# Performance work log

Hardware: AMD Instinct MI355X
Metric: run time of the kernel (lower is better)

The kernel has to match this reference:

```python
import jax, jax.numpy as jnp
import numpy as np

N_NODES = 100000
N_EDGES = 3200000
IN_FEATS = 16
OUT_FEATS = 2
K = 3


def setup_inputs() -> dict:
    key = jax.random.key(0)
    k1, k2, k3, k4 = jax.random.split(key, 4)
    in_feat = jax.random.normal(k1, (N_NODES, IN_FEATS), dtype=jnp.float32)
    # Linear(K*in_feats -> out_feats, bias=False) weight, torch layout (out, in)
    W = jax.random.normal(k2, (OUT_FEATS, K * IN_FEATS), dtype=jnp.float32) * (1.0 / np.sqrt(K * IN_FEATS))
    src = jax.random.randint(k3, (N_EDGES,), 0, N_NODES, dtype=jnp.int64)
    dst = jax.random.randint(k4, (N_EDGES,), 0, N_NODES, dtype=jnp.int64)
    # cached dgl.laplacian_lambda_max value; 2.0 is the normalized-Laplacian bound
    lambda_max = jnp.full((1,), 2.0, dtype=jnp.float32)
    return {"in_feat": in_feat, "W": W, "src": src, "dst": dst, "lambda_max": lambda_max}


def reference(in_feat, W, src, dst, lambda_max):
    N = in_feat.shape[0]
    # in-degree based symmetric normalization, clamp(min=1)
    deg = jax.ops.segment_sum(jnp.ones_like(dst, dtype=in_feat.dtype), dst, num_segments=N)
    norm = jnp.clip(deg, 1.0) ** -0.5  # (N,)
    norm = norm[:, None]
    re_norm = (2.0 / lambda_max)[None, :]  # (1,1), broadcasts over nodes

    def prop(x):
        # D^{-1/2} A D^{-1/2} x via gather from src, scatter-sum to dst
        m = (x * norm)[src]                                    # (E, d)
        return jax.ops.segment_sum(m, dst, num_segments=N) * norm

    X0 = in_feat
    X1 = -re_norm * prop(X0) + X0 * (re_norm - 1.0)
    X2 = -2.0 * re_norm * prop(X1) + X1 * (2.0 * (re_norm - 1.0)) - X0
    Xt = jnp.concatenate([X0, X1, X2], axis=1)                 # (N, K*d)
    h = Xt @ W.T                                               # (N, out)
    return jax.nn.relu(h)  # DGL ChebConv default activation
```

## Files before the change

kernel.cpp:

```cpp
#include <hip/hip_runtime.h>
#include <hip/hip_bf16.h>


#define NN   100000
#define NE   3200000
#define F    16
#define CB   128
#define NBUK 782
#define ECHK 8192
#define NBLK 391
#define LCAP 5120
#define HXW  1025
#define PCAP 4608

__device__ __forceinline__ float bflo(unsigned int u) {
    return __uint_as_float(u << 16);
}
__device__ __forceinline__ float bfhi(unsigned int u) {
    return __uint_as_float(u & 0xffff0000u);
}
__device__ __forceinline__ unsigned int f2bf(float f) {
    __hip_bfloat16 b = __float2bfloat16(f);
    return (unsigned int)*reinterpret_cast<unsigned short*>(&b);
}

__global__ __launch_bounds__(512) void k_lsort(const int* __restrict__ src,
        const int* __restrict__ dst, int* __restrict__ hxg, int* __restrict__ csort) {
    __shared__ int pk[ECHK];
    __shared__ int hx[HXW];
    __shared__ int cur[1024];
    __shared__ int csum[512];
    int t = threadIdx.x, blk = blockIdx.x;
    for (int j = t; j < 1024; j += 512) hx[j] = 0;
    __syncthreads();
    int s0 = blk * ECHK;
    int lim = min(s0 + ECHK, NE);
    for (int e = s0 + t; e < lim; e += 512)
        atomicAdd(&hx[dst[e] >> 7], 1);
    __syncthreads();
    int b0 = t * 2;
    int c0 = hx[b0], c1 = hx[b0 + 1];
    csum[t] = c0 + c1;
    __syncthreads();
    for (int o = 1; o < 512; o <<= 1) {
        int add = (t >= o) ? csum[t - o] : 0;
        __syncthreads();
        csum[t] += add;
        __syncthreads();
    }
    int ce = csum[t] - (c0 + c1);
    hx[b0] = ce;  hx[b0 + 1] = ce + c0;
    cur[b0] = ce; cur[b0 + 1] = ce + c0;
    if (t == 511) hx[1024] = csum[511];
    __syncthreads();
    for (int j = t; j < HXW; j += 512)
        hxg[blk * HXW + j] = hx[j];
    for (int e = s0 + t; e < lim; e += 512) {
        int d = dst[e];
        int pos = atomicAdd(&cur[d >> 7], 1);
        pk[pos] = (src[e] << 7) | (d & 127);
    }
    __syncthreads();
    int len = lim - s0;
    for (int i = t; i < len; i += 512)
        csort[s0 + i] = pk[i];
}

__global__ __launch_bounds__(512) void k_sort(const int* __restrict__ csort,
        const int* __restrict__ hxg, const float* __restrict__ X0,
        int* __restrict__ es, unsigned int* __restrict__ P,
        unsigned short* __restrict__ Y0, unsigned short* __restrict__ Y1) {
    __shared__ int pk[LCAP];
    __shared__ int pk2[LCAP];
    __shared__ int dsc[512];
    __shared__ int cnt[CB], loc[CB], cur[CB];
    __shared__ float nvs[CB];
    int b = blockIdx.x, t = threadIdx.x;
    int h0 = 0, c = 0;
    if (t < NBLK) {
        h0 = hxg[t * HXW + b];
        c  = hxg[t * HXW + b + 1] - h0;
    }
    dsc[t] = c;
    if (t < CB) cnt[t] = 0;
    if (b == 0 && t < 4) {
        ((uint2*)Y0)[(size_t)NN * 4 + t] = make_uint2(0u, 0u);
        ((uint2*)Y1)[(size_t)NN * 4 + t] = make_uint2(0u, 0u);
    }
    __syncthreads();
    for (int o = 1; o < 512; o <<= 1) {
        int add = (t >= o) ? dsc[t - o] : 0;
        __syncthreads();
        dsc[t] += add;
        __syncthreads();
    }
    int len = dsc[511];
    int dpos = dsc[t] - c;
    if (len > LCAP) len = LCAP;
    if (c > 0 && dpos < LCAP) {
        int rl = c;
        if (dpos + rl > LCAP) rl = LCAP - dpos;
        int sbase = t * ECHK + h0;
        for (int i = 0; i < rl; ++i)
            pk[dpos + i] = csort[sbase + i];
    }
    __syncthreads();
    for (int i = t; i < len; i += 512)
        atomicAdd(&cnt[pk[i] & 127], 1);
    __syncthreads();
    if (t < CB) loc[t] = cnt[t];
    __syncthreads();
    for (int o = 1; o < CB; o <<= 1) {
        int add = 0;
        if (t < CB && t >= o) add = loc[t - o];
        __syncthreads();
        if (t < CB) loc[t] += add;
        __syncthreads();
    }
    if (t < CB) {
        int excl = loc[t] - cnt[t];
        loc[t] = excl;
        cur[t] = excl;
        int n = b * CB + t;
        if (n < NN) {
            unsigned dg = cnt[t] > 1023 ? 1023u : (unsigned)cnt[t];
            P[n] = ((unsigned)(b * LCAP + excl) << 10) | dg;
            nvs[t] = rsqrtf((float)(cnt[t] < 1 ? 1 : cnt[t]));
        }
    }
    __syncthreads();
    for (int j = t; j < CB * 4; j += 512) {
        int dl = j >> 2;
        int n = b * CB + dl;
        if (n < NN) {
            float nv = nvs[dl];
            size_t g4 = (size_t)n * 4 + (j & 3);
            float4 x0 = ((const float4*)X0)[g4];
            uint2 o;
            o.x = f2bf(x0.x * nv) | (f2bf(x0.y * nv) << 16);
            o.y = f2bf(x0.z * nv) | (f2bf(x0.w * nv) << 16);
            ((uint2*)Y0)[g4] = o;
        }
    }
    for (int i = t; i < len; i += 512) {
        int p = pk[i];
        int pos = atomicAdd(&cur[p & 127], 1);
        pk2[pos] = p >> 7;
    }
    __syncthreads();
    for (int i = t; i < len; i += 512)
        es[b * LCAP + i] = pk2[i];
}

__global__ __launch_bounds__(256) void k_prop1(const unsigned int* __restrict__ P,
        const int* __restrict__ es, const unsigned short* __restrict__ Y0,
        const float* __restrict__ X0, const float* __restrict__ lm,
        unsigned short* __restrict__ Y1) {
    __shared__ int sidx[PCAP];
    int blk = blockIdx.x, t = threadIdx.x;
    int b = blk >> 1, half = blk & 1;
    int n0 = b * CB + half * 64;
    if (n0 >= NN) return;
    unsigned pk0 = P[n0];
    int nL = min(n0 + 63, NN - 1);
    unsigned pkL = P[nL];
    int st = (int)(pk0 >> 10);
    int en = (int)(pkL >> 10) + (int)(pkL & 1023u);
    int slen = en - st;
    if (slen > PCAP) slen = PCAP;
    for (int i = t; i < slen; i += 256)
        sidx[i] = es[st + i];
    __syncthreads();
    int n = n0 + (t >> 2), h = t & 3;
    if (n >= NN) return;
    unsigned pkn = P[n];
    int beg = (int)(pkn >> 10) - st;
    int dg = (int)(pkn & 1023u);
    int lend = min(beg + dg, slen);
    const uint2* Yv = (const uint2*)Y0;
    float a0 = 0.f, a1 = 0.f, a2 = 0.f, a3 = 0.f;
    for (int e0 = beg; e0 < lend; e0 += 8) {
#pragma unroll
        for (int j = 0; j < 8; ++j) {
            int sp = e0 + j;
            int s = (sp < lend) ? sidx[sp] : NN;
            uint2 u = Yv[(size_t)s * 4 + h];
            a0 += bflo(u.x); a1 += bfhi(u.x);
            a2 += bflo(u.y); a3 += bfhi(u.y);
        }
    }
    float nv = rsqrtf((float)(dg < 1 ? 1 : dg));
    float r  = 2.0f / lm[0];
    float k1 = -r * nv, k2 = r - 1.0f;
    int tid4 = n * 4 + h;
    float4 x0 = ((const float4*)X0)[tid4];
    float x1a = k1 * a0 + k2 * x0.x;
    float x1b = k1 * a1 + k2 * x0.y;
    float x1c = k1 * a2 + k2 * x0.z;
    float x1d = k1 * a3 + k2 * x0.w;
    uint2 o;
    o.x = f2bf(nv * x1a) | (f2bf(nv * x1b) << 16);
    o.y = f2bf(nv * x1c) | (f2bf(nv * x1d) << 16);
    ((uint2*)Y1)[tid4] = o;
}

__global__ __launch_bounds__(256) void k_prop2(const unsigned int* __restrict__ P,
        const int* __restrict__ es, const unsigned short* __restrict__ Y1,
        const float* __restrict__ X0, const float* __restrict__ lm,
        const float* __restrict__ W, float* __restrict__ out) {
    __shared__ int sidx[PCAP];
    __shared__ float Ws[96];
    int blk = blockIdx.x, t = threadIdx.x;
    int b = blk >> 1, half = blk & 1;
    int n0 = b * CB + half * 64;
    if (n0 >= NN) return;
    if (t < 96) Ws[t] = W[t];
    unsigned pk0 = P[n0];
    int nL = min(n0 + 63, NN - 1);
    unsigned pkL = P[nL];
    int st = (int)(pk0 >> 10);
    int en = (int)(pkL >> 10) + (int)(pkL & 1023u);
    int slen = en - st;
    if (slen > PCAP) slen = PCAP;
    for (int i = t; i < slen; i += 256)
        sidx[i] = es[st + i];
    __syncthreads();
    int n = n0 + (t >> 2), h = t & 3;
    if (n >= NN) return;
    unsigned pkn = P[n];
    int beg = (int)(pkn >> 10) - st;
    int dg = (int)(pkn & 1023u);
    int lend = min(beg + dg, slen);
    const uint2* Yv = (const uint2*)Y1;
    float a0 = 0.f, a1 = 0.f, a2 = 0.f, a3 = 0.f;
    for (int e0 = beg; e0 < lend; e0 += 8) {
#pragma unroll
        for (int j = 0; j < 8; ++j) {
            int sp = e0 + j;
            int s = (sp < lend) ? sidx[sp] : NN;
            uint2 u = Yv[(size_t)s * 4 + h];
            a0 += bflo(u.x); a1 += bfhi(u.x);
            a2 += bflo(u.y); a3 += bfhi(u.y);
        }
    }
    int dc = dg < 1 ? 1 : dg;
    float nv = rsqrtf((float)dc);
    float rn = sqrtf((float)dc);
    float r  = 2.0f / lm[0];
    int tid4 = n * 4 + h;
    float4 x0 = ((const float4*)X0)[tid4];
    uint2 uy = ((const uint2*)Y1)[tid4];
    float x1a = bflo(uy.x) * rn, x1b = bfhi(uy.x) * rn;
    float x1c = bflo(uy.y) * rn, x1d = bfhi(uy.y) * rn;
    float c1 = -2.0f * r * nv, c2 = 2.0f * (r - 1.0f);
    float x2a = c1 * a0 + c2 * x1a - x0.x;
    float x2b = c1 * a1 + c2 * x1b - x0.y;
    float x2c = c1 * a2 + c2 * x1c - x0.z;
    float x2d = c1 * a3 + c2 * x1d - x0.w;
    int f0 = 4 * h;
    float t0 = Ws[f0] * x0.x + Ws[f0 + 1] * x0.y + Ws[f0 + 2] * x0.z + Ws[f0 + 3] * x0.w
             + Ws[16 + f0] * x1a + Ws[17 + f0] * x1b + Ws[18 + f0] * x1c + Ws[19 + f0] * x1d
             + Ws[32 + f0] * x2a + Ws[33 + f0] * x2b + Ws[34 + f0] * x2c + Ws[35 + f0] * x2d;
    float t1 = Ws[48 + f0] * x0.x + Ws[49 + f0] * x0.y + Ws[50 + f0] * x0.z + Ws[51 + f0] * x0.w
             + Ws[64 + f0] * x1a + Ws[65 + f0] * x1b + Ws[66 + f0] * x1c + Ws[67 + f0] * x1d
             + Ws[80 + f0] * x2a + Ws[81 + f0] * x2b + Ws[82 + f0] * x2c + Ws[83 + f0] * x2d;
    t0 += __shfl_xor(t0, 2, 4); t0 += __shfl_xor(t0, 1, 4);
    t1 += __shfl_xor(t1, 2, 4); t1 += __shfl_xor(t1, 1, 4);
    if (h == 0) {
        out[(size_t)n * 2 + 0] = fmaxf(t0, 0.f);
        out[(size_t)n * 2 + 1] = fmaxf(t1, 0.f);
    }
}

extern "C" void kernel_launch(void* const* d_in, const int* in_sizes, int n_in,
                              void* d_out, int out_size, void* d_ws, size_t ws_size,
                              hipStream_t stream) {
    const float* X0  = (const float*)d_in[0];
    const float* W   = (const float*)d_in[1];
    const int*   src = (const int*)d_in[2];
    const int*   dst = (const int*)d_in[3];
    const float* lm  = (const float*)d_in[4];
    float* out = (float*)d_out;

    int*   hxg   = (int*)d_ws;
    int*   csort = hxg + (size_t)NBLK * HXW;
    int*   es    = csort + NE;
    unsigned int* P = (unsigned int*)(es + (size_t)NBUK * LCAP);
    unsigned short* Y0 = (unsigned short*)(P + NN);
    unsigned short* Y1 = Y0 + (size_t)(NN + 1) * F;

    k_lsort<<<NBLK, 512, 0, stream>>>(src, dst, hxg, csort);
    k_sort <<<NBUK, 512, 0, stream>>>(csort, hxg, X0, es, P, Y0, Y1);
    k_prop1<<<NBUK * 2, 256, 0, stream>>>(P, es, Y0, X0, lm, Y1);
    k_prop2<<<NBUK * 2, 256, 0, stream>>>(P, es, Y1, X0, lm, W, out);
}
```

Measured before the change: 175.1 us.

## Pad per-node edge lists to multiples of eight and vectorize index loads

Each node's sorted source list is now padded to a multiple of 8 with a sentinel index that points at a zero row, and offsets are stored in units of 8. The propagation kernels can then read indices as two int4 loads per group of 8 with no bounds checks. The sort kernel also drops the intermediate shared staging buffer and the 512-wide scan, reading csort twice directly from global memory instead. The costs are extra padded gather work, a larger LCAP footprint, and serial per-thread loops over csort.

```diff
diff --git a/kernel.cpp b/kernel.cpp
--- a/kernel.cpp
+++ b/kernel.cpp
@@ -9,7 +9,7 @@
 #define NBUK 782
 #define ECHK 8192
 #define NBLK 391
-#define LCAP 5120
+#define LCAP 5632
 #define HXW  1025
 #define PCAP 4608
 
@@ -70,45 +70,29 @@
         const int* __restrict__ hxg, const float* __restrict__ X0,
         int* __restrict__ es, unsigned int* __restrict__ P,
         unsigned short* __restrict__ Y0, unsigned short* __restrict__ Y1) {
-    __shared__ int pk[LCAP];
     __shared__ int pk2[LCAP];
-    __shared__ int dsc[512];
     __shared__ int cnt[CB], loc[CB], cur[CB];
     __shared__ float nvs[CB];
     int b = blockIdx.x, t = threadIdx.x;
-    int h0 = 0, c = 0;
-    if (t < NBLK) {
-        h0 = hxg[t * HXW + b];
-        c  = hxg[t * HXW + b + 1] - h0;
-    }
-    dsc[t] = c;
     if (t < CB) cnt[t] = 0;
     if (b == 0 && t < 4) {
         ((uint2*)Y0)[(size_t)NN * 4 + t] = make_uint2(0u, 0u);
         ((uint2*)Y1)[(size_t)NN * 4 + t] = make_uint2(0u, 0u);
     }
-    __syncthreads();
-    for (int o = 1; o < 512; o <<= 1) {
-        int add = (t >= o) ? dsc[t - o] : 0;
-        __syncthreads();
-        dsc[t] += add;
-        __syncthreads();
-    }
-    int len = dsc[511];
-    int dpos = dsc[t] - c;
-    if (len > LCAP) len = LCAP;
-    if (c > 0 && dpos < LCAP) {
-        int rl = c;
-        if (dpos + rl > LCAP) rl = LCAP - dpos;
-        int sbase = t * ECHK + h0;
-        for (int i = 0; i < rl; ++i)
-            pk[dpos + i] = csort[sbase + i];
-    }
-    __syncthreads();
-    for (int i = t; i < len; i += 512)
-        atomicAdd(&cnt[pk[i] & 127], 1);
-    __syncthreads();
-    if (t < CB) loc[t] = cnt[t];
+    int h0 = 0, rl = 0;
+    if (t < NBLK) {
+        h0 = hxg[t * HXW + b];
+        rl = hxg[t * HXW + b + 1] - h0;
+    }
+    int sbase = t * ECHK + h0;
+    __syncthreads();
+    for (int i = 0; i < rl; ++i) {
+        int p = csort[sbase + i];
+        atomicAdd(&cnt[p & 127], 1);
+    }
+    __syncthreads();
+    int pc = 0;
+    if (t < CB) { pc = (cnt[t] + 7) & ~7; loc[t] = pc; }
     __syncthreads();
     for (int o = 1; o < CB; o <<= 1) {
         int add = 0;
@@ -118,17 +102,29 @@
         __syncthreads();
     }
     if (t < CB) {
-        int excl = loc[t] - cnt[t];
+        int excl = loc[t] - pc;
         loc[t] = excl;
         cur[t] = excl;
         int n = b * CB + t;
         if (n < NN) {
-            unsigned dg = cnt[t] > 1023 ? 1023u : (unsigned)cnt[t];
-            P[n] = ((unsigned)(b * LCAP + excl) << 10) | dg;
+            unsigned dgc = cnt[t] > 1023 ? 1023u : (unsigned)cnt[t];
+            P[n] = ((unsigned)((b * LCAP + excl) >> 3) << 10) | dgc;
             nvs[t] = rsqrtf((float)(cnt[t] < 1 ? 1 : cnt[t]));
         }
     }
     __syncthreads();
+    int plen = loc[CB - 1] + ((cnt[CB - 1] + 7) & ~7);
+    if (plen > LCAP) plen = LCAP;
+    if (t < CB) {
+        int e0 = loc[t] + cnt[t];
+        int e1 = loc[t] + ((cnt[t] + 7) & ~7);
+        for (int i = e0; i < e1 && i < LCAP; ++i) pk2[i] = NN;
+    }
+    for (int i = 0; i < rl; ++i) {
+        int p = csort[sbase + i];
+        int pos = atomicAdd(&cur[p & 127], 1);
+        if (pos < LCAP) pk2[pos] = p >> 7;
+    }
     for (int j = t; j < CB * 4; j += 512) {
         int dl = j >> 2;
         int n = b * CB + dl;
@@ -142,13 +138,8 @@
             ((uint2*)Y0)[g4] = o;
         }
     }
-    for (int i = t; i < len; i += 512) {
-        int p = pk[i];
-        int pos = atomicAdd(&cur[p & 127], 1);
-        pk2[pos] = p >> 7;
-    }
-    __syncthreads();
-    for (int i = t; i < len; i += 512)
+    __syncthreads();
+    for (int i = t; i < plen; i += 512)
         es[b * LCAP + i] = pk2[i];
 }
 
@@ -156,7 +147,7 @@
         const int* __restrict__ es, const unsigned short* __restrict__ Y0,
         const float* __restrict__ X0, const float* __restrict__ lm,
         unsigned short* __restrict__ Y1) {
-    __shared__ int sidx[PCAP];
+    __shared__ __align__(16) int sidx[PCAP];
     int blk = blockIdx.x, t = threadIdx.x;
     int b = blk >> 1, half = blk & 1;
     int n0 = b * CB + half * 64;
@@ -164,8 +155,8 @@
     unsigned pk0 = P[n0];
     int nL = min(n0 + 63, NN - 1);
     unsigned pkL = P[nL];
-    int st = (int)(pk0 >> 10);
-    int en = (int)(pkL >> 10) + (int)(pkL & 1023u);
+    int st = (int)(pk0 >> 10) << 3;
+    int en = ((int)(pkL >> 10) << 3) + (int)(((pkL & 1023u) + 7u) & ~7u);
     int slen = en - st;
     if (slen > PCAP) slen = PCAP;
     for (int i = t; i < slen; i += 256)
@@ -174,20 +165,20 @@
     int n = n0 + (t >> 2), h = t & 3;
     if (n >= NN) return;
     unsigned pkn = P[n];
-    int beg = (int)(pkn >> 10) - st;
+    int beg = ((int)(pkn >> 10) << 3) - st;
     int dg = (int)(pkn & 1023u);
-    int lend = min(beg + dg, slen);
+    int nb = (dg + 7) >> 3;
     const uint2* Yv = (const uint2*)Y0;
     float a0 = 0.f, a1 = 0.f, a2 = 0.f, a3 = 0.f;
-    for (int e0 = beg; e0 < lend; e0 += 8) {
-#pragma unroll
-        for (int j = 0; j < 8; ++j) {
-            int sp = e0 + j;
-            int s = (sp < lend) ? sidx[sp] : NN;
-            uint2 u = Yv[(size_t)s * 4 + h];
-            a0 += bflo(u.x); a1 += bfhi(u.x);
-            a2 += bflo(u.y); a3 += bfhi(u.y);
-        }
+    for (int bb = 0; bb < nb; ++bb) {
+        int e0 = beg + bb * 8;
+        int4 ia = *(const int4*)&sidx[e0];
+        int4 ib = *(const int4*)&sidx[e0 + 4];
+#define ACC(S) { uint2 u = Yv[(size_t)(S) * 4 + h]; \
+                 a0 += bflo(u.x); a1 += bfhi(u.x); \
+                 a2 += bflo(u.y); a3 += bfhi(u.y); }
+        ACC(ia.x) ACC(ia.y) ACC(ia.z) ACC(ia.w)
+        ACC(ib.x) ACC(ib.y) ACC(ib.z) ACC(ib.w)
     }
     float nv = rsqrtf((float)(dg < 1 ? 1 : dg));
     float r  = 2.0f / lm[0];
@@ -208,7 +199,7 @@
         const int* __restrict__ es, const unsigned short* __restrict__ Y1,
         const float* __restrict__ X0, const float* __restrict__ lm,
         const float* __restrict__ W, float* __restrict__ out) {
-    __shared__ int sidx[PCAP];
+    __shared__ __align__(16) int sidx[PCAP];
     __shared__ float Ws[96];
     int blk = blockIdx.x, t = threadIdx.x;
     int b = blk >> 1, half = blk & 1;
@@ -218,8 +209,8 @@
     unsigned pk0 = P[n0];
     int nL = min(n0 + 63, NN - 1);
     unsigned pkL = P[nL];
-    int st = (int)(pk0 >> 10);
-    int en = (int)(pkL >> 10) + (int)(pkL & 1023u);
+    int st = (int)(pk0 >> 10) << 3;
+    int en = ((int)(pkL >> 10) << 3) + (int)(((pkL & 1023u) + 7u) & ~7u);
     int slen = en - st;
     if (slen > PCAP) slen = PCAP;
     for (int i = t; i < slen; i += 256)
@@ -228,20 +219,17 @@
     int n = n0 + (t >> 2), h = t & 3;
     if (n >= NN) return;
     unsigned pkn = P[n];
-    int beg = (int)(pkn >> 10) - st;
+    int beg = ((int)(pkn >> 10) << 3) - st;
     int dg = (int)(pkn & 1023u);
-    int lend = min(beg + dg, slen);
+    int nb = (dg + 7) >> 3;
     const uint2* Yv = (const uint2*)Y1;
     float a0 = 0.f, a1 = 0.f, a2 = 0.f, a3 = 0.f;
-    for (int e0 = beg; e0 < lend; e0 += 8) {
-#pragma unroll
-        for (int j = 0; j < 8; ++j) {
-            int sp = e0 + j;
-            int s = (sp < lend) ? sidx[sp] : NN;
-            uint2 u = Yv[(size_t)s * 4 + h];
-            a0 += bflo(u.x); a1 += bfhi(u.x);
-            a2 += bflo(u.y); a3 += bfhi(u.y);
-        }
+    for (int bb = 0; bb < nb; ++bb) {
+        int e0 = beg + bb * 8;
+        int4 ia = *(const int4*)&sidx[e0];
+        int4 ib = *(const int4*)&sidx[e0 + 4];
+        ACC(ia.x) ACC(ia.y) ACC(ia.z) ACC(ia.w)
+        ACC(ib.x) ACC(ib.y) ACC(ib.z) ACC(ib.w)
     }
     int dc = dg < 1 ? 1 : dg;
     float nv = rsqrtf((float)dc);
```

Result: slower. 190.1 us (+8.6%).
